# Kernel optimization log

Measured on AMD Instinct MI355X. Metric: run time of the kernel, lower is better.

Reference implementation:

```python
import jax, jax.numpy as jnp
import numpy as np

N_QUBITS = 4
Q_DEPTH = 6
Q_DELTA = 0.01
INPUT_SIZE = 64
BATCH = 262144


def _ry_gate(theta):
    # RY(theta) = [[cos(t/2), -sin(t/2)], [sin(t/2), cos(t/2)]]; theta scalar or (B,)
    c = jnp.cos(theta / 2)
    s = jnp.sin(theta / 2)
    return jnp.stack([jnp.stack([c, -s], -1), jnp.stack([s, c], -1)], -2)


def _apply_1q(state, gate, wire):
    # state: (B,2,2,2,2); gate: (2,2) shared or (B,2,2) per-sample
    ax = wire + 1
    s = jnp.moveaxis(state, ax, -1)
    if gate.ndim == 2:
        s = jnp.einsum('ij,b...j->b...i', gate, s)
    else:
        s = jnp.einsum('bij,b...j->b...i', gate, s)
    return jnp.moveaxis(s, -1, ax)


def _apply_cnot(state, ctrl, tgt):
    ca, ta = ctrl + 1, tgt + 1
    s0 = jnp.take(state, jnp.array([0]), axis=ca)
    s1 = jnp.take(state, jnp.array([1]), axis=ca)
    s1 = jnp.flip(s1, axis=ta)  # X on target where control=1
    return jnp.concatenate([s0, s1], axis=ca)


def _quantum_net(q_in, q_weights):
    # q_in: (B, 4) per-sample RY angles; q_weights: (Q_DEPTH, 4)
    B = q_in.shape[0]
    # H layer on |0000>: uniform real amplitude 1/4 over all 16 basis states
    state = jnp.full((B,) + (2,) * N_QUBITS, 0.25, dtype=q_in.dtype)
    for w in range(N_QUBITS):
        state = _apply_1q(state, _ry_gate(q_in[:, w]), w)
    for k in range(Q_DEPTH):
        for i in range(0, N_QUBITS - 1, 2):
            state = _apply_cnot(state, i, i + 1)
        for i in range(1, N_QUBITS - 1, 2):
            state = _apply_cnot(state, i, i + 1)
        for w in range(N_QUBITS):
            state = _apply_1q(state, _ry_gate(q_weights[k, w]), w)
    # All gates are real -> real statevector; probs = amp^2
    probs = state * state
    signs = jnp.array([1.0, -1.0], dtype=state.dtype)
    expz = []
    for w in range(N_QUBITS):
        shp = [1] * (N_QUBITS + 1)
        shp[w + 1] = 2
        expz.append(jnp.sum(probs * signs.reshape(shp), axis=tuple(range(1, N_QUBITS + 1))))
    return jnp.stack(expz, axis=-1)  # (B, 4)


def setup_inputs() -> dict:
    key = jax.random.key(0)
    k1, k2, k3, k4, k5, k6 = jax.random.split(key, 6)
    bound_pre = 1.0 / np.sqrt(INPUT_SIZE)
    bound_post = 1.0 / np.sqrt(N_QUBITS)
    return {
        'input_features': jax.random.normal(k1, (BATCH, INPUT_SIZE), dtype=jnp.float32),
        'pre_w': jax.random.uniform(k2, (N_QUBITS, INPUT_SIZE), jnp.float32, -bound_pre, bound_pre),
        'pre_b': jax.random.uniform(k3, (N_QUBITS,), jnp.float32, -bound_pre, bound_pre),
        'q_params': Q_DELTA * jax.random.normal(k4, (Q_DEPTH * N_QUBITS,), dtype=jnp.float32),
        'post_w': jax.random.uniform(k5, (1, N_QUBITS), jnp.float32, -bound_post, bound_post),
        'post_b': jax.random.uniform(k6, (1,), jnp.float32, -bound_post, bound_post),
    }


def reference(input_features, pre_w, pre_b, q_params, post_w, post_b):
    pre_out = input_features @ pre_w.T + pre_b
    q_in = jnp.tanh(pre_out) * (jnp.pi / 2.0)
    q_out = _quantum_net(q_in, q_params.reshape(Q_DEPTH, N_QUBITS))
    return q_out @ post_w.T + post_b  # (B, 1)
```

## Files before the change

### kernel.cpp

```cpp
#include <hip/hip_runtime.h>
#include <math.h>

#define NQ      4
#define QDEPTH  6
#define TPB     256
#define ROWLEN  64

__device__ __forceinline__ float fast_tanh(float x) {
    float e = __expf(2.0f * x);
    float r = __builtin_amdgcn_rcpf(e + 1.0f);
    return fmaf(-2.0f, r, 1.0f);
}

template<int W>
__device__ __forceinline__ void apply_ry(float st[16], float c, float s) {
    constexpr int M = 8 >> W;
#pragma unroll
    for (int i = 0; i < 16; ++i) {
        if ((i & M) == 0) {
            float a0 = st[i];
            float a1 = st[i | M];
            st[i]     = fmaf(c, a0, -(s * a1));
            st[i | M] = fmaf(s, a0,  (c * a1));
        }
    }
}

template<int C, int T>
__device__ __forceinline__ void apply_cnot(float st[16]) {
    constexpr int MC = 8 >> C;
    constexpr int MT = 8 >> T;
#pragma unroll
    for (int i = 0; i < 16; ++i) {
        if ((i & MC) != 0 && (i & MT) == 0) {
            float tmp = st[i];
            st[i] = st[i | MT];
            st[i | MT] = tmp;
        }
    }
}

__global__ __launch_bounds__(TPB, 4) void dqnet_kernel(
    const float* __restrict__ inp,
    const float* __restrict__ pre_w,
    const float* __restrict__ pre_b,
    const float* __restrict__ qp,
    const float* __restrict__ post_w,
    const float* __restrict__ post_b,
    float* __restrict__ out)
{
    __shared__ float cw[QDEPTH * NQ];
    __shared__ float sw[QDEPTH * NQ];
    __shared__ float gg[16];

    const int t = threadIdx.x;

    if (t < QDEPTH * NQ) {
        float h = 0.5f * qp[t];
        cw[t] = __cosf(h);
        sw[t] = __sinf(h);
    } else if (t >= 32 && t < 48) {
        int i = t - 32;
        float v = 0.0f;
#pragma unroll
        for (int w = 0; w < NQ; ++w) {
            float p = post_w[w];
            v += ((i >> (3 - w)) & 1) ? -p : p;
        }
        gg[i] = v;
    }
    __syncthreads();

    const size_t row = (size_t)blockIdx.x * TPB + t;
    const float4* rp  = (const float4*)(inp + row * ROWLEN);
    const float4* pw4 = (const float4*)pre_w;

    float acc0 = pre_b[0], acc1 = pre_b[1], acc2 = pre_b[2], acc3 = pre_b[3];
#pragma unroll
    for (int i = 0; i < 16; ++i) {
        float4 x  = rp[i];
        float4 w0 = pw4[i];
        float4 w1 = pw4[16 + i];
        float4 w2 = pw4[32 + i];
        float4 w3 = pw4[48 + i];
        acc0 = fmaf(x.x, w0.x, acc0); acc0 = fmaf(x.y, w0.y, acc0);
        acc0 = fmaf(x.z, w0.z, acc0); acc0 = fmaf(x.w, w0.w, acc0);
        acc1 = fmaf(x.x, w1.x, acc1); acc1 = fmaf(x.y, w1.y, acc1);
        acc1 = fmaf(x.z, w1.z, acc1); acc1 = fmaf(x.w, w1.w, acc1);
        acc2 = fmaf(x.x, w2.x, acc2); acc2 = fmaf(x.y, w2.y, acc2);
        acc2 = fmaf(x.z, w2.z, acc2); acc2 = fmaf(x.w, w2.w, acc2);
        acc3 = fmaf(x.x, w3.x, acc3); acc3 = fmaf(x.y, w3.y, acc3);
        acc3 = fmaf(x.z, w3.z, acc3); acc3 = fmaf(x.w, w3.w, acc3);
    }

    const float QK = 0.78539816339744831f;
    float h0 = fast_tanh(acc0) * QK;
    float h1 = fast_tanh(acc1) * QK;
    float h2 = fast_tanh(acc2) * QK;
    float h3 = fast_tanh(acc3) * QK;
    float c0 = __cosf(h0), s0 = __sinf(h0);
    float c1 = __cosf(h1), s1 = __sinf(h1);
    float c2 = __cosf(h2), s2 = __sinf(h2);
    float c3 = __cosf(h3), s3 = __sinf(h3);

    const float R = 0.70710678118654752f;
    float u0 = (c0 - s0) * R, v0 = (c0 + s0) * R;
    float u1 = (c1 - s1) * R, v1 = (c1 + s1) * R;
    float u2 = (c2 - s2) * R, v2 = (c2 + s2) * R;
    float u3 = (c3 - s3) * R, v3 = (c3 + s3) * R;

    float p00 = u0 * u1, p01 = u0 * v1, p10 = v0 * u1, p11 = v0 * v1;
    float q00 = u2 * u3, q01 = u2 * v3, q10 = v2 * u3, q11 = v2 * v3;

    float st[16];
    st[ 0] = p00 * q00; st[ 1] = p00 * q01; st[ 2] = p00 * q10; st[ 3] = p00 * q11;
    st[ 4] = p01 * q00; st[ 5] = p01 * q01; st[ 6] = p01 * q10; st[ 7] = p01 * q11;
    st[ 8] = p10 * q00; st[ 9] = p10 * q01; st[10] = p10 * q10; st[11] = p10 * q11;
    st[12] = p11 * q00; st[13] = p11 * q01; st[14] = p11 * q10; st[15] = p11 * q11;

#pragma unroll
    for (int k = 0; k < QDEPTH; ++k) {
        apply_cnot<0, 1>(st);
        apply_cnot<2, 3>(st);
        apply_cnot<1, 2>(st);
        apply_ry<0>(st, cw[k * 4 + 0], sw[k * 4 + 0]);
        apply_ry<1>(st, cw[k * 4 + 1], sw[k * 4 + 1]);
        apply_ry<2>(st, cw[k * 4 + 2], sw[k * 4 + 2]);
        apply_ry<3>(st, cw[k * 4 + 3], sw[k * 4 + 3]);
    }

    float r = post_b[0];
#pragma unroll
    for (int i = 0; i < 16; ++i)
        r = fmaf(st[i] * st[i], gg[i], r);

    out[row] = r;
}

extern "C" void kernel_launch(void* const* d_in, const int* in_sizes, int n_in,
                              void* d_out, int out_size, void* d_ws, size_t ws_size,
                              hipStream_t stream) {
    const float* inp    = (const float*)d_in[0];
    const float* pre_w  = (const float*)d_in[1];
    const float* pre_b  = (const float*)d_in[2];
    const float* qp     = (const float*)d_in[3];
    const float* post_w = (const float*)d_in[4];
    const float* post_b = (const float*)d_in[5];
    float* out = (float*)d_out;

    int n = in_sizes[0] / ROWLEN;
    int grid = n / TPB;
    dqnet_kernel<<<grid, TPB, 0, stream>>>(inp, pre_w, pre_b, qp, post_w, post_b, out);
}
```

Before: 104.8 us.

## Stage input rows through swizzled LDS tile for coalesced global loads

Each wave now loads its 64 input rows cooperatively, with lanes reading adjacent float4s so the global loads coalesce, instead of each thread streaming its own 256-byte row. The rows go into an XOR-swizzled shared-memory tile in two halves and are then read back per thread to form the dot products. This targets poor memory coalescing of the row-per-thread pattern. The cost is 32KB of LDS per block, which may limit occupancy, plus extra LDS traffic. There is no barrier between the LDS writes and reads; that relies on each wave owning its own tile region and on wave-level execution order.

```diff
diff --git a/kernel.cpp b/kernel.cpp
--- a/kernel.cpp
+++ b/kernel.cpp
@@ -49,6 +49,7 @@
     const float* __restrict__ post_b,
     float* __restrict__ out)
 {
+    __shared__ float4 tile[4 * 512];
     __shared__ float cw[QDEPTH * NQ];
     __shared__ float sw[QDEPTH * NQ];
     __shared__ float gg[16];
@@ -71,18 +72,64 @@
     }
     __syncthreads();
 
-    const size_t row = (size_t)blockIdx.x * TPB + t;
-    const float4* rp  = (const float4*)(inp + row * ROWLEN);
+    const int wave = t >> 6;
+    const int lane = t & 63;
+    const size_t wrow0 = (size_t)blockIdx.x * TPB + wave * 64;
+    const float4* gp = (const float4*)(inp + wrow0 * ROWLEN);
+    float4* wt = &tile[wave * 512];
     const float4* pw4 = (const float4*)pre_w;
 
+    float4 x0[8], x1[8];
+#pragma unroll
+    for (int j = 0; j < 8; ++j) {
+        int idx = j * 64 + lane;
+        int rw = idx >> 3, c = idx & 7;
+        x0[j] = gp[rw * 16 + c];
+    }
+#pragma unroll
+    for (int j = 0; j < 8; ++j) {
+        int idx = j * 64 + lane;
+        int rw = idx >> 3, c = idx & 7;
+        wt[rw * 8 + (c ^ (rw & 7))] = x0[j];
+    }
+#pragma unroll
+    for (int j = 0; j < 8; ++j) {
+        int idx = j * 64 + lane;
+        int rw = idx >> 3, c = idx & 7;
+        x1[j] = gp[rw * 16 + 8 + c];
+    }
+
     float acc0 = pre_b[0], acc1 = pre_b[1], acc2 = pre_b[2], acc3 = pre_b[3];
 #pragma unroll
-    for (int i = 0; i < 16; ++i) {
-        float4 x  = rp[i];
-        float4 w0 = pw4[i];
-        float4 w1 = pw4[16 + i];
-        float4 w2 = pw4[32 + i];
-        float4 w3 = pw4[48 + i];
+    for (int i = 0; i < 8; ++i) {
+        float4 x  = wt[lane * 8 + (i ^ (lane & 7))];
+        float4 w0 = pw4[0 * 16 + i];
+        float4 w1 = pw4[1 * 16 + i];
+        float4 w2 = pw4[2 * 16 + i];
+        float4 w3 = pw4[3 * 16 + i];
+        acc0 = fmaf(x.x, w0.x, acc0); acc0 = fmaf(x.y, w0.y, acc0);
+        acc0 = fmaf(x.z, w0.z, acc0); acc0 = fmaf(x.w, w0.w, acc0);
+        acc1 = fmaf(x.x, w1.x, acc1); acc1 = fmaf(x.y, w1.y, acc1);
+        acc1 = fmaf(x.z, w1.z, acc1); acc1 = fmaf(x.w, w1.w, acc1);
+        acc2 = fmaf(x.x, w2.x, acc2); acc2 = fmaf(x.y, w2.y, acc2);
+        acc2 = fmaf(x.z, w2.z, acc2); acc2 = fmaf(x.w, w2.w, acc2);
+        acc3 = fmaf(x.x, w3.x, acc3); acc3 = fmaf(x.y, w3.y, acc3);
+        acc3 = fmaf(x.z, w3.z, acc3); acc3 = fmaf(x.w, w3.w, acc3);
+    }
+
+#pragma unroll
+    for (int j = 0; j < 8; ++j) {
+        int idx = j * 64 + lane;
+        int rw = idx >> 3, c = idx & 7;
+        wt[rw * 8 + (c ^ (rw & 7))] = x1[j];
+    }
+#pragma unroll
+    for (int i = 0; i < 8; ++i) {
+        float4 x  = wt[lane * 8 + (i ^ (lane & 7))];
+        float4 w0 = pw4[0 * 16 + 8 + i];
+        float4 w1 = pw4[1 * 16 + 8 + i];
+        float4 w2 = pw4[2 * 16 + 8 + i];
+        float4 w3 = pw4[3 * 16 + 8 + i];
         acc0 = fmaf(x.x, w0.x, acc0); acc0 = fmaf(x.y, w0.y, acc0);
         acc0 = fmaf(x.z, w0.z, acc0); acc0 = fmaf(x.w, w0.w, acc0);
         acc1 = fmaf(x.x, w1.x, acc1); acc1 = fmaf(x.y, w1.y, acc1);
@@ -134,7 +181,7 @@
     for (int i = 0; i < 16; ++i)
         r = fmaf(st[i] * st[i], gg[i], r);
 
-    out[row] = r;
+    out[wrow0 + lane] = r;
 }
 
 extern "C" void kernel_launch(void* const* d_in, const int* in_sizes, int n_in,
```

Result: faster. 101.8 us (-2.9%).
